# Kernel optimization log

Hardware: AMD Instinct MI355X
Metric: run time of the kernel (lower is better)

## Reference

```python
import jax, jax.numpy as jnp
import numpy as np
from jax import lax

N = 2048
P = 256
F_J = 0.05      # sparsity of recurrent matrix J
F_OUT = 0.05    # sparsity of readout
DT = 0.1
ON_TIME = 10
T = 200


def _activation(x):
    # Tanh_shifted_and_scaled: rates in [0, 1]
    return 0.5 * (1.0 + jnp.tanh(x))


def setup_inputs() -> dict:
    key = jax.random.key(0)
    k1, k2, k3, k4, k5 = jax.random.split(key, 5)
    # patterns ~ Uniform(-1, 1), shape [N, P]
    patterns = jax.random.uniform(k1, (N, P), jnp.float32, -1.0, 1.0)
    # sparse recurrent matrix J: gaussian values, density F_J, gain g
    g = 10.0 * 0.1 ** 0.25 / np.sqrt(N * P * np.sqrt(F_J))
    J_dense = jax.random.normal(k2, (N, N), jnp.float32) * jnp.float32(g)
    mask = jax.random.uniform(k3, (N, N)) < F_J
    J = jnp.where(mask, J_dense, 0.0).astype(jnp.float32)
    # sparse readout: ones at a random F_OUT fraction of units (frozen)
    w_out = (jax.random.uniform(k4, (N,)) < F_OUT).astype(jnp.float32)
    return {"patterns": patterns, "J": J, "w_out": w_out, "N_time_steps": T}


def reference(patterns, J, w_out, N_time_steps):
    # Batched over all P patterns at once (columns of [N, P] state).
    n = patterns.shape[0]
    x0 = jnp.zeros_like(patterns)           # [N, P]
    r0 = _activation(x0)

    def step(carry, ti):
        x, rates = carry
        inp = jnp.where(ti < ON_TIME, patterns, 0.0)      # [N, P]
        x = x + DT * (-x + J @ rates + inp)               # [N, P]
        rates = _activation(x)
        out_t = w_out @ rates                             # [P]
        return (x, rates), out_t

    _, outs = lax.scan(step, (x0, r0), jnp.arange(N_time_steps))  # [T, P]
    readout = outs.T / n                                   # [P, T]
    return readout
```

## Files before the change

### kernel.cpp

```cpp
#include <hip/hip_runtime.h>
#include <hip/hip_bf16.h>


#define NN 2048
#define PP 256
#define DT_C 0.1f
#define ON_TIME_C 10

typedef __attribute__((ext_vector_type(8)))  short bf16x8;
typedef __attribute__((ext_vector_type(16))) float f32x16;

__device__ __forceinline__ unsigned short bf16rne(float f) {
    unsigned b = __float_as_uint(f);
    return (unsigned short)((b + 0x7FFFu + ((b >> 16) & 1u)) >> 16);
}
__device__ __forceinline__ int kperm16(int s) {
    return (s & 3) + (((s >> 2) & 1) << 3) + ((s >> 3) << 2);
}

__global__ void convert_J_kernel(const float* __restrict__ J,
                                 unsigned short* __restrict__ Jp) {
    int i = blockIdx.x * blockDim.x + threadIdx.x;
    int row = i >> 11, k = i & 2047;
    Jp[((size_t)row << 11) + (k & ~15) + kperm16(k & 15)] = bf16rne(J[i]);
}

__global__ void init_kernel(float* __restrict__ x,
                            unsigned short* __restrict__ rT,
                            float* __restrict__ out, int nout) {
    int i = blockIdx.x * blockDim.x + threadIdx.x;
    x[i] = 0.0f;
    rT[i] = 0x3F00;
    if (i < nout) out[i] = 0.0f;
}

#define AS1 __attribute__((address_space(1)))
#define AS3 __attribute__((address_space(3)))
#define GLOAD16(g, l) \
    __builtin_amdgcn_global_load_lds((const AS1 void*)(g), (AS3 void*)(l), 16, 0, 0)

__global__ __launch_bounds__(512, 1) void gemm_step_kernel(
    const unsigned short* __restrict__ Jp,
    const unsigned short* __restrict__ rin,
    unsigned short* __restrict__ rout,
    float* __restrict__ x, const float* __restrict__ patterns,
    const float* __restrict__ w_out, float* __restrict__ out,
    int t, int T, int with_input) {

    __shared__ char smem[147456];

    const int tid  = threadIdx.x;
    const int w    = tid >> 6;
    const int lane = tid & 63;
    const int s    = w >> 2;
    const int kq   = w & 3;
    const int h    = lane >> 5;

    const int bid   = (blockIdx.x & 7) * 32 + (blockIdx.x >> 3);
    const int mbase = (bid >> 3) * 64;
    const int nbase = (bid & 7) * 32;

    const int rA0 = 8 * w + (lane >> 4);
    const int rA1 = rA0 + 4;
    const int rB  = 4 * w + (lane >> 4);
    const char* gA0 = (const char*)Jp  + (((size_t)(mbase + rA0)) << 12)
                      + (((lane & 15) ^ (rA0 & 15)) << 4);
    const char* gA1 = (const char*)Jp  + (((size_t)(mbase + rA1)) << 12)
                      + (((lane & 15) ^ (rA1 & 15)) << 4);
    const char* gB  = (const char*)rin + (((size_t)(nbase + rB )) << 12)
                      + (((lane & 15) ^ (rB  & 15)) << 4);
    const int ldsA0 = (8 * w) * 256, ldsA1 = (8 * w + 4) * 256;
    const int ldsB  = 16384 + 4 * w * 256;

    const int rA  = 32 * s + (lane & 31);
    const int rBn = lane & 31;

    const int e_s2 = tid >> 8, e_rr = (tid >> 3) & 31, e_c4 = (tid & 7) * 4;
    const int e_mloc = e_s2 * 32 + e_rr;
    const int e_m  = mbase + e_mloc;
    const int e_n0 = nbase + e_c4;
    const size_t e_xo = ((size_t)e_m << 8) + e_n0;
    float4 e_xv = *(const float4*)(x + e_xo);
    float4 e_pv = make_float4(0.f, 0.f, 0.f, 0.f);
    if (with_input) e_pv = *(const float4*)(patterns + e_xo);
    float e_wsc = (w_out[e_m] != 0.0f) ? (1.0f / (float)NN) : 0.0f;

    f32x16 acc = {};

    #pragma unroll
    for (int ps = 0; ps < 4; ++ps) {
        GLOAD16(gA0 + ps * 256, smem + ps * 24576 + ldsA0);
        GLOAD16(gA1 + ps * 256, smem + ps * 24576 + ldsA1);
        GLOAD16(gB  + ps * 256, smem + ps * 24576 + ldsB);
    }

    #pragma unroll
    for (int ph = 0; ph < 16; ++ph) {
        if (ph < 12) {
            const int bo = ((ph + 4) % 6) * 24576;
            GLOAD16(gA0 + (ph + 4) * 256, smem + bo + ldsA0);
            GLOAD16(gA1 + (ph + 4) * 256, smem + bo + ldsA1);
            GLOAD16(gB  + (ph + 4) * 256, smem + bo + ldsB);
        }
        if (ph < 12)       asm volatile("s_waitcnt vmcnt(12)" ::: "memory");
        else if (ph == 12) asm volatile("s_waitcnt vmcnt(9)"  ::: "memory");
        else if (ph == 13) asm volatile("s_waitcnt vmcnt(6)"  ::: "memory");
        else if (ph == 14) asm volatile("s_waitcnt vmcnt(3)"  ::: "memory");
        else               asm volatile("s_waitcnt vmcnt(0)"  ::: "memory");
        __builtin_amdgcn_s_barrier();
        __builtin_amdgcn_sched_barrier(0);

        const int bb = (ph % 6) * 24576;
        #pragma unroll
        for (int sl = 0; sl < 2; ++sl) {
            const int c = kq * 4 + sl * 2 + h;
            bf16x8 a = *(const bf16x8*)(smem + bb + rA * 256
                                        + ((c ^ (rA & 15)) << 4));
            bf16x8 b = *(const bf16x8*)(smem + bb + 16384 + rBn * 256
                                        + ((c ^ (rBn & 15)) << 4));
            acc = __builtin_amdgcn_mfma_f32_32x32x16_bf16(a, b, acc, 0, 0, 0);
        }
    }

    __syncthreads();

    {
        float* pf = (float*)smem;
        const int plane = (s * 4 + kq) * 1024;
        #pragma unroll
        for (int reg = 0; reg < 16; ++reg) {
            int row = (reg & 3) + 8 * (reg >> 2) + 4 * h;
            pf[plane + row * 32 + (lane & 31)] = acc[reg];
        }
    }
    __syncthreads();

    {
        const float4* pf4 = (const float4*)smem;
        int base = ((e_s2 * 4) * 1024 + e_rr * 32 + e_c4) >> 2;
        float4 v0 = pf4[base], v1 = pf4[base + 256];
        float4 v2 = pf4[base + 512], v3 = pf4[base + 768];
        float sum[4] = {v0.x + v1.x + v2.x + v3.x, v0.y + v1.y + v2.y + v3.y,
                        v0.z + v1.z + v2.z + v3.z, v0.w + v1.w + v2.w + v3.w};

        float xn[4] = {e_xv.x + DT_C * (sum[0] + e_pv.x - e_xv.x),
                       e_xv.y + DT_C * (sum[1] + e_pv.y - e_xv.y),
                       e_xv.z + DT_C * (sum[2] + e_pv.z - e_xv.z),
                       e_xv.w + DT_C * (sum[3] + e_pv.w - e_xv.w)};
        *(float4*)(x + e_xo) = make_float4(xn[0], xn[1], xn[2], xn[3]);

        const int pos = (e_mloc & ~15) + kperm16(e_mloc & 15);
        #pragma unroll
        for (int j = 0; j < 4; ++j) {
            float r = 0.5f * (1.0f + tanhf(xn[j]));
            if (e_wsc != 0.0f)
                atomicAdd(&out[(size_t)(e_n0 + j) * T + t], r * e_wsc);
            int nloc = e_c4 + j;
            int byte = 32768 + nloc * 128
                     + (((pos >> 3) ^ (nloc & 7)) << 4) + (pos & 7) * 2;
            *(unsigned short*)(smem + byte) = bf16rne(r);
        }
    }
    __syncthreads();
    if (tid < 256) {
        int nl = tid >> 3, pc = tid & 7;
        uint4 v = *(const uint4*)(smem + 32768 + nl * 128 + ((pc ^ (nl & 7)) << 4));
        *(uint4*)((char*)rout + (((size_t)(nbase + nl)) << 12) + mbase * 2 + pc * 16) = v;
    }
}

extern "C" void kernel_launch(void* const* d_in, const int* in_sizes, int n_in,
                              void* d_out, int out_size, void* d_ws, size_t ws_size,
                              hipStream_t stream) {
    const float* patterns = (const float*)d_in[0];
    const float* J        = (const float*)d_in[1];
    const float* w_out    = (const float*)d_in[2];
    float* out            = (float*)d_out;

    int T = out_size / PP;

    size_t off = 0;
    auto alloc = [&](size_t bytes) {
        void* p = (char*)d_ws + off;
        off += (bytes + 255) & ~(size_t)255;
        return p;
    };
    unsigned short* Jp = (unsigned short*)alloc((size_t)NN * NN * 2);
    unsigned short* r0 = (unsigned short*)alloc((size_t)PP * NN * 2);
    unsigned short* r1 = (unsigned short*)alloc((size_t)PP * NN * 2);
    float*          x  = (float*)         alloc((size_t)NN * PP * 4);
    (void)ws_size; (void)n_in; (void)in_sizes;

    convert_J_kernel<<<(NN * NN) / 256, 256, 0, stream>>>(J, Jp);
    init_kernel<<<(NN * PP) / 256, 256, 0, stream>>>(x, r0, out, PP * T);

    for (int t = 0; t < T; ++t) {
        const unsigned short* rin = (t & 1) ? r1 : r0;
        unsigned short*      rout = (t & 1) ? r0 : r1;
        gemm_step_kernel<<<256, 512, 0, stream>>>(Jp, rin, rout, x, patterns,
                                                  w_out, out, t, T,
                                                  (t < ON_TIME_C) ? 1 : 0);
    }
}
```

Baseline: 1.942 ms.

## Double K-chunk size per phase and switch to triple-buffered LDS pipeline

```diff
diff --git a/kernel.cpp b/kernel.cpp
--- a/kernel.cpp
+++ b/kernel.cpp
@@ -60,17 +60,25 @@
     const int mbase = (bid >> 3) * 64;
     const int nbase = (bid & 7) * 32;
 
-    const int rA0 = 8 * w + (lane >> 4);
-    const int rA1 = rA0 + 4;
-    const int rB  = 4 * w + (lane >> 4);
-    const char* gA0 = (const char*)Jp  + (((size_t)(mbase + rA0)) << 12)
-                      + (((lane & 15) ^ (rA0 & 15)) << 4);
-    const char* gA1 = (const char*)Jp  + (((size_t)(mbase + rA1)) << 12)
-                      + (((lane & 15) ^ (rA1 & 15)) << 4);
-    const char* gB  = (const char*)rin + (((size_t)(nbase + rB )) << 12)
-                      + (((lane & 15) ^ (rB  & 15)) << 4);
-    const int ldsA0 = (8 * w) * 256, ldsA1 = (8 * w + 4) * 256;
-    const int ldsB  = 16384 + 4 * w * 256;
+    const int p32 = lane & 31;
+    const char* gA[4]; int ldsA[4];
+    #pragma unroll
+    for (int j = 0; j < 4; ++j) {
+        int li   = w * 4 + j;
+        int arow = 2 * li + (lane >> 5);
+        gA[j] = (const char*)Jp + (((size_t)(mbase + arow)) << 12)
+                + ((p32 ^ (arow & 15)) << 4);
+        ldsA[j] = li * 1024;
+    }
+    const char* gB[2]; int ldsB[2];
+    #pragma unroll
+    for (int j = 0; j < 2; ++j) {
+        int li   = w * 2 + j;
+        int brow = 2 * li + (lane >> 5);
+        gB[j] = (const char*)rin + (((size_t)(nbase + brow)) << 12)
+                + ((p32 ^ (brow & 15)) << 4);
+        ldsB[j] = 32768 + li * 1024;
+    }
 
     const int rA  = 32 * s + (lane & 31);
     const int rBn = lane & 31;
@@ -88,35 +96,37 @@
     f32x16 acc = {};
 
     #pragma unroll
-    for (int ps = 0; ps < 4; ++ps) {
-        GLOAD16(gA0 + ps * 256, smem + ps * 24576 + ldsA0);
-        GLOAD16(gA1 + ps * 256, smem + ps * 24576 + ldsA1);
-        GLOAD16(gB  + ps * 256, smem + ps * 24576 + ldsB);
-    }
-
-    #pragma unroll
-    for (int ph = 0; ph < 16; ++ph) {
-        if (ph < 12) {
-            const int bo = ((ph + 4) % 6) * 24576;
-            GLOAD16(gA0 + (ph + 4) * 256, smem + bo + ldsA0);
-            GLOAD16(gA1 + (ph + 4) * 256, smem + bo + ldsA1);
-            GLOAD16(gB  + (ph + 4) * 256, smem + bo + ldsB);
-        }
-        if (ph < 12)       asm volatile("s_waitcnt vmcnt(12)" ::: "memory");
-        else if (ph == 12) asm volatile("s_waitcnt vmcnt(9)"  ::: "memory");
-        else if (ph == 13) asm volatile("s_waitcnt vmcnt(6)"  ::: "memory");
-        else if (ph == 14) asm volatile("s_waitcnt vmcnt(3)"  ::: "memory");
-        else               asm volatile("s_waitcnt vmcnt(0)"  ::: "memory");
+    for (int ps = 0; ps < 2; ++ps) {
+        const int bo = ps * 49152;
+        #pragma unroll
+        for (int j = 0; j < 4; ++j) GLOAD16(gA[j] + ps * 512, smem + bo + ldsA[j]);
+        #pragma unroll
+        for (int j = 0; j < 2; ++j) GLOAD16(gB[j] + ps * 512, smem + bo + ldsB[j]);
+    }
+
+    #pragma unroll
+    for (int ph = 0; ph < 8; ++ph) {
+        if (ph < 7) asm volatile("s_waitcnt vmcnt(6)" ::: "memory");
+        else        asm volatile("s_waitcnt vmcnt(0)" ::: "memory");
         __builtin_amdgcn_s_barrier();
+        if (ph < 6) {
+            const int bo = ((ph + 2) % 3) * 49152;
+            #pragma unroll
+            for (int j = 0; j < 4; ++j)
+                GLOAD16(gA[j] + (ph + 2) * 512, smem + bo + ldsA[j]);
+            #pragma unroll
+            for (int j = 0; j < 2; ++j)
+                GLOAD16(gB[j] + (ph + 2) * 512, smem + bo + ldsB[j]);
+        }
         __builtin_amdgcn_sched_barrier(0);
 
-        const int bb = (ph % 6) * 24576;
-        #pragma unroll
-        for (int sl = 0; sl < 2; ++sl) {
-            const int c = kq * 4 + sl * 2 + h;
-            bf16x8 a = *(const bf16x8*)(smem + bb + rA * 256
+        const int bb = (ph % 3) * 49152;
+        #pragma unroll
+        for (int sl = 0; sl < 4; ++sl) {
+            const int c = kq * 8 + sl * 2 + h;
+            bf16x8 a = *(const bf16x8*)(smem + bb + rA * 512
                                         + ((c ^ (rA & 15)) << 4));
-            bf16x8 b = *(const bf16x8*)(smem + bb + 16384 + rBn * 256
+            bf16x8 b = *(const bf16x8*)(smem + bb + 32768 + rBn * 512
                                         + ((c ^ (rBn & 15)) << 4));
             acc = __builtin_amdgcn_mfma_f32_32x32x16_bf16(a, b, acc, 0, 0, 0);
         }
```

Result: slower. 2.002 ms (+3.1%).
